# Optimization experiments

Hardware: AMD Instinct MI355X
Metric: run time of the kernel (lower is better)

The kernel has to match this reference:

```python
import jax, jax.numpy as jnp
import numpy as np

D_MODEL = 1024
N_HEADS = 16
HEAD_DIM = D_MODEL // N_HEADS
ROPE_BASE = 10000.0


def rotate_half(x):
    x1, x2 = x[..., : x.shape[-1] // 2], x[..., x.shape[-1] // 2 :]
    return jnp.concatenate((-x2, x1), axis=-1)


def rope_cos_sin(L, dim, dtype):
    inv_freq = 1.0 / (ROPE_BASE ** (jnp.arange(0, dim, 2, dtype=jnp.float32) / dim))
    freqs = jnp.arange(L, dtype=jnp.float32)[:, None] * inv_freq[None, :]  # [L, dim/2]
    emb = jnp.concatenate((freqs, freqs), axis=-1)  # [L, dim]
    # broadcast over batch and heads: [1, L, 1, dim]
    return jnp.cos(emb)[None, :, None, :].astype(dtype), jnp.sin(emb)[None, :, None, :].astype(dtype)


def setup_inputs() -> dict:
    key = jax.random.key(0)
    ks = jax.random.split(key, 11)
    N, L, S = 2, 2048, 2048
    s = 1.0 / np.sqrt(D_MODEL)
    return {
        "queries": jax.random.normal(ks[0], (N, L, D_MODEL), jnp.float32),
        "keys": jax.random.normal(ks[1], (N, S, D_MODEL), jnp.float32),
        "values": jax.random.normal(ks[2], (N, S, D_MODEL), jnp.float32),
        "Wq": jax.random.normal(ks[3], (D_MODEL, D_MODEL), jnp.float32) * s,
        "bq": jnp.zeros((D_MODEL,), jnp.float32),
        "Wk": jax.random.normal(ks[4], (D_MODEL, D_MODEL), jnp.float32) * s,
        "bk": jnp.zeros((D_MODEL,), jnp.float32),
        "Wv": jax.random.normal(ks[5], (D_MODEL, D_MODEL), jnp.float32) * s,
        "bv": jnp.zeros((D_MODEL,), jnp.float32),
        "Wo": jax.random.normal(ks[6], (D_MODEL, D_MODEL), jnp.float32) * s,
        "bo": jnp.zeros((D_MODEL,), jnp.float32),
    }


def reference(queries, keys, values, Wq, bq, Wk, bk, Wv, bv, Wo, bo):
    N, L, _ = queries.shape
    S = keys.shape[1]
    H, hd = N_HEADS, HEAD_DIM

    # QKV projections (nn.Linear: x @ W.T + b), reshape to [N, T, H, hd]
    q = (jnp.einsum("nld,ed->nle", queries, Wq) + bq).reshape(N, L, H, hd)
    k = (jnp.einsum("nsd,ed->nse", keys, Wk) + bk).reshape(N, S, H, hd)
    v = (jnp.einsum("nsd,ed->nse", values, Wv) + bv).reshape(N, S, H, hd)

    # Rotary embedding: q*cos + rotate_half(q)*sin  (same for k)
    cos, sin = rope_cos_sin(L, hd, q.dtype)
    q = q * cos + rotate_half(q) * sin
    k = k * cos + rotate_half(k) * sin

    # Inner attention: scaled dot-product with causal mask
    scores = jnp.einsum("nlhd,nshd->nhls", q, k) / jnp.sqrt(jnp.asarray(hd, q.dtype))
    causal = jnp.tril(jnp.ones((L, S), bool))
    scores = jnp.where(causal[None, None], scores, jnp.asarray(-1e9, scores.dtype))
    attn = jax.nn.softmax(scores, axis=-1)
    out = jnp.einsum("nhls,nshd->nlhd", attn, v).reshape(N, L, H * hd)

    # Output projection
    return jnp.einsum("nle,de->nld", out, Wo) + bo
```

## Files before the change

### kernel.cpp

```cpp
#include <hip/hip_runtime.h>
#include <math.h>

#define DM 1024
#define NH 16
#define HD 64
#define SEQ 2048
#define NB2 2
#define MROWS 4096

typedef unsigned short u16;
typedef __attribute__((ext_vector_type(8))) short short8;
typedef __attribute__((ext_vector_type(4))) float f32x4;
typedef __attribute__((ext_vector_type(2))) unsigned int u32x2;

#define GLOAD16(g, l) __builtin_amdgcn_global_load_lds( \
    (const __attribute__((address_space(1))) void*)(g),  \
    (__attribute__((address_space(3))) void*)(l), 16, 0, 0)

static __device__ __forceinline__ u16 f2bf(float f) {
  union { float f; unsigned u; } v; v.f = f;
  unsigned r = v.u + 0x7fffu + ((v.u >> 16) & 1u);
  return (u16)(r >> 16);
}

static __device__ __forceinline__ short8 cvt8(float4 a, float4 b) {
  short8 s;
  s[0] = (short)f2bf(a.x); s[1] = (short)f2bf(a.y);
  s[2] = (short)f2bf(a.z); s[3] = (short)f2bf(a.w);
  s[4] = (short)f2bf(b.x); s[5] = (short)f2bf(b.y);
  s[6] = (short)f2bf(b.z); s[7] = (short)f2bf(b.w);
  return s;
}

__global__ void conv_all(
    const float* __restrict__ q, const float* __restrict__ k, const float* __restrict__ v,
    const float* __restrict__ wq, const float* __restrict__ wk,
    const float* __restrict__ wv, const float* __restrict__ wo,
    u16* __restrict__ xq, u16* __restrict__ xk, u16* __restrict__ xv,
    u16* __restrict__ wqb, u16* __restrict__ wkb, u16* __restrict__ wvb, u16* __restrict__ wob,
    float* __restrict__ cosT, float* __restrict__ sinT)
{
  const int z = blockIdx.z;
  const int idx = blockIdx.x * blockDim.x + threadIdx.x;
  if (z == 7) {
    if (idx >= SEQ * 32) return;
    int l = idx >> 5, i = idx & 31;
    float invf = expf(-(float)i * (9.210340371976184f / 32.0f));
    float ang = (float)l * invf;
    float s, c;
    sincosf(ang, &s, &c);
    cosT[idx] = c; sinT[idx] = s;
    return;
  }
  const float* src; u16* dst; int n;
  switch (z) {
    case 0: src = q;  dst = xq;  n = MROWS * DM; break;
    case 1: src = k;  dst = xk;  n = MROWS * DM; break;
    case 2: src = v;  dst = xv;  n = MROWS * DM; break;
    case 3: src = wq; dst = wqb; n = DM * DM; break;
    case 4: src = wk; dst = wkb; n = DM * DM; break;
    case 5: src = wv; dst = wvb; n = DM * DM; break;
    default: src = wo; dst = wob; n = DM * DM; break;
  }
  const int base = idx * 8;
  if (base >= n) return;
  float4 a = *(const float4*)(src + base);
  float4 b = *(const float4*)(src + base + 4);
  *(short8*)(dst + base) = cvt8(a, b);
}

#define VSTR 136
template<int EPI>
__device__ __forceinline__ void gemm_body(
    u16* SH,
    const u16* __restrict__ A, const u16* __restrict__ W,
    const float* __restrict__ bias,
    u16* __restrict__ Cb, float* __restrict__ Cf, u16* __restrict__ VT,
    const float* __restrict__ cosT, const float* __restrict__ sinT,
    float qscale, int row0, int col0)
{
  const int tid = threadIdx.x;
  const int lane = tid & 63;
  const int wid = tid >> 6;
  const int wr = wid & 3;
  const int wc = wid >> 2;
  const int fr = lane & 15, kg = lane >> 4;

  const u16* ga = A + (size_t)(row0 + (tid & 127)) * DM + ((tid >> 7) << 3);
  const u16* gb = W + (size_t)(col0 + (tid & 127)) * DM + ((tid >> 7) << 3);
  const int lw = wid * 512;
  u16* B0 = SH;
  u16* B1 = SH + 16384;

  f32x4 acc[2][4];
#pragma unroll
  for (int m = 0; m < 2; ++m)
#pragma unroll
    for (int n = 0; n < 4; ++n) acc[m][n] = (f32x4){0.f, 0.f, 0.f, 0.f};

  auto issue = [&](int t, u16* buf) {
    const int ko = t * 64;
    GLOAD16(ga + ko, buf + lw);
    GLOAD16(ga + ko + 32, buf + lw + 4096);
    GLOAD16(gb + ko, buf + 8192 + lw);
    GLOAD16(gb + ko + 32, buf + 8192 + lw + 4096);
  };
  auto compute = [&](const u16* buf, int kk) {
    const int kc = kk * 4 + kg;
    short8 afr[2], bfr[4];
#pragma unroll
    for (int m = 0; m < 2; ++m)
      afr[m] = *(const short8*)(&buf[kc * 1024 + (wr * 32 + m * 16 + fr) * 8]);
#pragma unroll
    for (int n = 0; n < 4; ++n)
      bfr[n] = *(const short8*)(&buf[8192 + kc * 1024 + (wc * 64 + n * 16 + fr) * 8]);
    __builtin_amdgcn_s_setprio(1);
#pragma unroll
    for (int m = 0; m < 2; ++m)
#pragma unroll
      for (int n = 0; n < 4; ++n)
        acc[m][n] = __builtin_amdgcn_mfma_f32_16x16x32_bf16(afr[m], bfr[n], acc[m][n], 0, 0, 0);
    __builtin_amdgcn_s_setprio(0);
  };

  issue(0, B0);
  const int KT = DM / 64;
  for (int t = 0; t < KT; ++t) {
    u16* bufR = (t & 1) ? B1 : B0;
    u16* bufW = (t & 1) ? B0 : B1;
    __syncthreads();
    if (t + 1 < KT) issue(t + 1, bufW);
    compute(bufR, 0);
    compute(bufR, 1);
  }

  if (EPI == 2) {
    __syncthreads();
    const int nb = row0 >> 11;
    const int sbase = row0 & (SEQ - 1);
#pragma unroll
    for (int p = 0; p < 2; ++p) {
      if (wc == p) {
#pragma unroll
        for (int n = 0; n < 4; ++n) {
          const int dcol = n * 16 + fr;
          const float bv = bias[col0 + p * 64 + dcol];
#pragma unroll
          for (int m = 0; m < 2; ++m)
#pragma unroll
            for (int r = 0; r < 4; ++r)
              SH[dcol * VSTR + wr * 32 + m * 16 + kg * 4 + r] = f2bf(acc[m][n][r] + bv);
        }
      }
      __syncthreads();
      {
        const int dcol = tid >> 3, sq = tid & 7;
        const int e = col0 + p * 64 + dcol;
        u16* dst = VT + ((size_t)(nb * NH + (e >> 6)) * HD + (e & 63)) * SEQ + sbase + sq * 16;
        *(short8*)(dst)     = *(const short8*)(&SH[dcol * VSTR + sq * 16]);
        *(short8*)(dst + 8) = *(const short8*)(&SH[dcol * VSTR + sq * 16 + 8]);
      }
      __syncthreads();
    }
    return;
  }

#pragma unroll
  for (int m = 0; m < 2; ++m) {
#pragma unroll
    for (int r = 0; r < 4; ++r) {
      const int rowg = row0 + wr * 32 + m * 16 + kg * 4 + r;
      if (EPI == 1) {
#pragma unroll
        for (int n = 0; n < 4; ++n) {
          const int colg = col0 + wc * 64 + n * 16 + fr;
          Cf[(size_t)rowg * DM + colg] = acc[m][n][r] + bias[colg];
        }
      } else {
        const int l = rowg & (SEQ - 1);
#pragma unroll
        for (int n = 0; n < 4; ++n) {
          const int colg = col0 + wc * 64 + n * 16 + fr;
          const int i = n * 16 + fr;
          const int fi = i & 31;
          const float c = cosT[l * 32 + fi];
          const float s = sinT[l * 32 + fi];
          const float v = acc[m][n][r] + bias[colg];
          const float pv = acc[m][n ^ 2][r] + bias[col0 + wc * 64 + ((n ^ 2) * 16 + fr)];
          const float o = v * c + ((i < 32) ? -pv : pv) * s;
          Cb[(size_t)rowg * DM + colg] = f2bf(o * qscale);
        }
      }
    }
  }
}

__global__ __launch_bounds__(512) void gemm_qkv(
    const u16* __restrict__ Xq, const u16* __restrict__ Xk, const u16* __restrict__ Xv,
    const u16* __restrict__ Wqb, const u16* __restrict__ Wkb, const u16* __restrict__ Wvb,
    const float* __restrict__ bq, const float* __restrict__ bk, const float* __restrict__ bv,
    u16* __restrict__ Qb, u16* __restrict__ Kb, u16* __restrict__ VT,
    const float* __restrict__ cosT, const float* __restrict__ sinT)
{
  __shared__ __align__(16) u16 SH[32768];
  const int z = blockIdx.z;
  const int row0 = blockIdx.x * 128, col0 = blockIdx.y * 128;
  if (z == 2) {
    gemm_body<2>(SH, Xv, Wvb, bv, nullptr, nullptr, VT, nullptr, nullptr, 1.0f, row0, col0);
  } else if (z == 0) {
    gemm_body<0>(SH, Xq, Wqb, bq, Qb, nullptr, nullptr, cosT, sinT, 0.125f, row0, col0);
  } else {
    gemm_body<0>(SH, Xk, Wkb, bk, Kb, nullptr, nullptr, cosT, sinT, 1.0f, row0, col0);
  }
}

__global__ __launch_bounds__(512) void gemm_o(
    const u16* __restrict__ Ob, const u16* __restrict__ Wob,
    const float* __restrict__ bo, float* __restrict__ out)
{
  __shared__ __align__(16) u16 SH[32768];
  gemm_body<1>(SH, Ob, Wob, bo, nullptr, out, nullptr, nullptr, nullptr, 1.0f,
               blockIdx.x * 128, blockIdx.y * 128);
}

__global__ __launch_bounds__(512) void flash_attn(
    const u16* __restrict__ Qp, const u16* __restrict__ Kp,
    const u16* __restrict__ VT, u16* __restrict__ Op)
{
  __shared__ __align__(16) u16 Ks[4096];
  __shared__ __align__(16) u16 Vt[4096];
  __shared__ __align__(16) u16 Pl[9216];

  const int tid = threadIdx.x;
  const int lane = tid & 63;
  const int w = tid >> 6;
  const int fr = lane & 15, rg = lane >> 4;
  const int qbp = blockIdx.x;
  const int h = blockIdx.y, nb = blockIdx.z;

  const size_t headoff = (size_t)nb * SEQ * DM + (size_t)h * HD;
  const size_t vthead = (size_t)(nb * NH + h) * HD * SEQ;
  const int srow = tid >> 3;
  const int sch  = tid & 7;
  u16* Pw = &Pl[w * 1152];

  for (int pass = 0; pass < 2; ++pass) {
    const int qe = pass ? (15 - qbp) : qbp;
    const int KBend = 2 * qe + 2;
    const int qrow0 = qe * 128 + w * 16;
    const int qg = qrow0 + fr;

    short8 qf[2];
#pragma unroll
    for (int ck = 0; ck < 2; ++ck)
      qf[ck] = *(const short8*)(Qp + headoff + (size_t)(qrow0 + fr) * DM + ck * 32 + rg * 8);

    f32x4 accO[4];
#pragma unroll
    for (int df = 0; df < 4; ++df) accO[df] = (f32x4){0.f, 0.f, 0.f, 0.f};
    float m_run = -3e38f, l_run = 0.f;

    short8 kpf = *(const short8*)(Kp + headoff + (size_t)srow * DM + sch * 8);
    short8 vpf = *(const short8*)(VT + vthead + (size_t)srow * SEQ + sch * 8);

    for (int kb = 0; kb < KBend; ++kb) {
      *(short8*)(&Ks[(sch * 64 + (srow ^ sch)) * 8]) = kpf;
      *(short8*)(&Vt[(sch * 64 + (srow ^ sch)) * 8]) = vpf;
      __syncthreads();
      if (kb + 1 < KBend) {
        kpf = *(const short8*)(Kp + headoff + (size_t)((kb + 1) * 64 + srow) * DM + sch * 8);
        vpf = *(const short8*)(VT + vthead + (size_t)srow * SEQ + (kb + 1) * 64 + sch * 8);
      }

      const bool active = (kb * 64) <= (qrow0 + 15);
      if (active) {
        short8 kf[4][2];
#pragma unroll
        for (int sf = 0; sf < 4; ++sf)
#pragma unroll
          for (int ck = 0; ck < 2; ++ck) {
            const int dc = ck * 4 + rg;
            kf[sf][ck] = *(const short8*)(&Ks[(dc * 64 + ((sf * 16 + fr) ^ dc)) * 8]);
          }
        f32x4 sc_[4];
#pragma unroll
        for (int sf = 0; sf < 4; ++sf) {
          f32x4 z = (f32x4){0.f, 0.f, 0.f, 0.f};
#pragma unroll
          for (int ck = 0; ck < 2; ++ck)
            z = __builtin_amdgcn_mfma_f32_16x16x32_bf16(kf[sf][ck], qf[ck], z, 0, 0, 0);
          sc_[sf] = z;
        }
        float rowmax = -3e38f;
#pragma unroll
        for (int sf = 0; sf < 4; ++sf)
#pragma unroll
          for (int r = 0; r < 4; ++r) {
            const int sg = kb * 64 + sf * 16 + rg * 4 + r;
            float v = sc_[sf][r];
            v = (sg <= qg) ? v : -3e38f;
            sc_[sf][r] = v;
            rowmax = fmaxf(rowmax, v);
          }
        rowmax = fmaxf(rowmax, __shfl_xor(rowmax, 16, 64));
        rowmax = fmaxf(rowmax, __shfl_xor(rowmax, 32, 64));
        const float mnew = fmaxf(m_run, rowmax);
        const float scl = __expf(m_run - mnew);
        m_run = mnew;
        float psum = 0.f;
#pragma unroll
        for (int sf = 0; sf < 4; ++sf)
#pragma unroll
          for (int r = 0; r < 4; ++r) {
            const float p = __expf(sc_[sf][r] - mnew);
            sc_[sf][r] = p;
            psum += p;
          }
        psum += __shfl_xor(psum, 16, 64);
        psum += __shfl_xor(psum, 32, 64);
        l_run = l_run * scl + psum;
        const float s0 = __shfl(scl, rg * 4 + 0, 64);
        const float s1 = __shfl(scl, rg * 4 + 1, 64);
        const float s2 = __shfl(scl, rg * 4 + 2, 64);
        const float s3 = __shfl(scl, rg * 4 + 3, 64);
#pragma unroll
        for (int df = 0; df < 4; ++df) {
          accO[df][0] *= s0; accO[df][1] *= s1;
          accO[df][2] *= s2; accO[df][3] *= s3;
        }
#pragma unroll
        for (int sf = 0; sf < 4; ++sf) {
          u32x2 pv;
          pv[0] = (unsigned)f2bf(sc_[sf][0]) | ((unsigned)f2bf(sc_[sf][1]) << 16);
          pv[1] = (unsigned)f2bf(sc_[sf][2]) | ((unsigned)f2bf(sc_[sf][3]) << 16);
          *(u32x2*)(&Pw[fr * 72 + (sf * 8 + rg * 2) * 2]) = pv;
        }
        short8 pa[2];
#pragma unroll
        for (int ck = 0; ck < 2; ++ck)
          pa[ck] = *(const short8*)(&Pw[fr * 72 + (ck * 16 + rg * 4) * 2]);
#pragma unroll
        for (int df = 0; df < 4; ++df)
#pragma unroll
          for (int ck = 0; ck < 2; ++ck) {
            const int sc = ck * 4 + rg;
            const short8 vf = *(const short8*)(&Vt[(sc * 64 + ((df * 16 + fr) ^ sc)) * 8]);
            accO[df] = __builtin_amdgcn_mfma_f32_16x16x32_bf16(pa[ck], vf, accO[df], 0, 0, 0);
          }
      }
      __syncthreads();
    }

    const float l0 = __shfl(l_run, rg * 4 + 0, 64);
    const float l1 = __shfl(l_run, rg * 4 + 1, 64);
    const float l2 = __shfl(l_run, rg * 4 + 2, 64);
    const float l3 = __shfl(l_run, rg * 4 + 3, 64);
#pragma unroll
    for (int df = 0; df < 4; ++df) {
      const int d = df * 16 + fr;
      Op[headoff + (size_t)(qrow0 + rg * 4 + 0) * DM + d] = f2bf(accO[df][0] / l0);
      Op[headoff + (size_t)(qrow0 + rg * 4 + 1) * DM + d] = f2bf(accO[df][1] / l1);
      Op[headoff + (size_t)(qrow0 + rg * 4 + 2) * DM + d] = f2bf(accO[df][2] / l2);
      Op[headoff + (size_t)(qrow0 + rg * 4 + 3) * DM + d] = f2bf(accO[df][3] / l3);
    }
  }
}

extern "C" void kernel_launch(void* const* d_in, const int* in_sizes, int n_in,
                              void* d_out, int out_size, void* d_ws, size_t ws_size,
                              hipStream_t stream) {
  (void)in_sizes; (void)n_in; (void)out_size; (void)ws_size;
  const float* queries = (const float*)d_in[0];
  const float* keys    = (const float*)d_in[1];
  const float* values  = (const float*)d_in[2];
  const float* Wq = (const float*)d_in[3];
  const float* bq = (const float*)d_in[4];
  const float* Wk = (const float*)d_in[5];
  const float* bk = (const float*)d_in[6];
  const float* Wv = (const float*)d_in[7];
  const float* bv = (const float*)d_in[8];
  const float* Wo = (const float*)d_in[9];
  const float* bo = (const float*)d_in[10];
  float* out = (float*)d_out;

  char* ws = (char*)d_ws;
  const size_t MB = 1u << 20;
  u16* Qb  = (u16*)(ws);
  u16* Kb  = (u16*)(ws + 8 * MB);
  u16* VTg = (u16*)(ws + 16 * MB);
  u16* Xq  = (u16*)(ws + 24 * MB);
  u16* Ob  = Xq;
  u16* Xk  = (u16*)(ws + 32 * MB);
  u16* Xv  = (u16*)(ws + 40 * MB);
  u16* Wqb = (u16*)(ws + 48 * MB);
  u16* Wkb = (u16*)(ws + 50 * MB);
  u16* Wvb = (u16*)(ws + 52 * MB);
  u16* Wob = (u16*)(ws + 54 * MB);
  float* cosT = (float*)(ws + 56 * MB);
  float* sinT = (float*)(ws + 56 * MB + 256 * 1024);

  conv_all<<<dim3(2048, 1, 8), 256, 0, stream>>>(
      queries, keys, values, Wq, Wk, Wv, Wo,
      Xq, Xk, Xv, Wqb, Wkb, Wvb, Wob, cosT, sinT);
  gemm_qkv<<<dim3(MROWS / 128, DM / 128, 3), 512, 0, stream>>>(
      Xq, Xk, Xv, Wqb, Wkb, Wvb, bq, bk, bv, Qb, Kb, VTg, cosT, sinT);
  flash_attn<<<dim3(SEQ / 256, NH, NB2), 512, 0, stream>>>(Qb, Kb, VTg, Ob);
  gemm_o<<<dim3(MROWS / 128, DM / 128), 512, 0, stream>>>(Ob, Wob, bo, out);
}
```

Before: 149.4 us.

## Use 256x256 tiles with triple-buffered LDS pipeline for QKV GEMM

The QKV projection kernel moves from 128x128 to 256x256 output tiles, with each wave computing 128x64 using 8x4 MFMA accumulators, and k-steps of 32. It adds a three-buffer global_load_lds pipeline with explicit vmcnt waits and raw s_barrier so two tiles stay in flight. The goal is more data reuse per LDS load and less global traffic. In exchange the grid shrinks to 16x4x3=192 blocks (below CU count), register pressure rises, and LDS use grows to 96KB.

```diff
diff --git a/kernel.cpp b/kernel.cpp
--- a/kernel.cpp
+++ b/kernel.cpp
@@ -69,16 +69,155 @@
   *(short8*)(dst + base) = cvt8(a, b);
 }
 
-#define VSTR 136
-template<int EPI>
-__device__ __forceinline__ void gemm_body(
-    u16* SH,
-    const u16* __restrict__ A, const u16* __restrict__ W,
-    const float* __restrict__ bias,
-    u16* __restrict__ Cb, float* __restrict__ Cf, u16* __restrict__ VT,
-    const float* __restrict__ cosT, const float* __restrict__ sinT,
-    float qscale, int row0, int col0)
+__global__ __launch_bounds__(512) void gemm_qkv(
+    const u16* __restrict__ Xq, const u16* __restrict__ Xk, const u16* __restrict__ Xv,
+    const u16* __restrict__ Wqb, const u16* __restrict__ Wkb, const u16* __restrict__ Wvb,
+    const float* __restrict__ bq, const float* __restrict__ bk, const float* __restrict__ bv,
+    u16* __restrict__ Qb, u16* __restrict__ Kb, u16* __restrict__ VT,
+    const float* __restrict__ cosT, const float* __restrict__ sinT)
 {
+  __shared__ __align__(16) u16 SH[49152];
+  const int z = blockIdx.z;
+  const u16* A = (z == 0) ? Xq : (z == 1) ? Xk : Xv;
+  const u16* W = (z == 0) ? Wqb : (z == 1) ? Wkb : Wvb;
+  const float* bias = (z == 0) ? bq : (z == 1) ? bk : bv;
+  const int row0 = blockIdx.x * 256, col0 = blockIdx.y * 256;
+
+  const int tid = threadIdx.x;
+  const int lane = tid & 63;
+  const int wid = tid >> 6;
+  const int wm = wid >> 2;
+  const int wn = wid & 3;
+  const int fr = lane & 15, kg = lane >> 4;
+
+  const u16* ga = A + (size_t)(row0 + (tid & 255)) * DM + ((tid >> 8) << 3);
+  const u16* gb = W + (size_t)(col0 + (tid & 255)) * DM + ((tid >> 8) << 3);
+  const int lw = (wid >> 2) * 2048 + (wid & 3) * 512;
+  u16* B0 = SH;
+  u16* B1 = SH + 16384;
+  u16* B2 = SH + 32768;
+
+  f32x4 acc[8][4];
+#pragma unroll
+  for (int m = 0; m < 8; ++m)
+#pragma unroll
+    for (int n = 0; n < 4; ++n) acc[m][n] = (f32x4){0.f, 0.f, 0.f, 0.f};
+
+  auto issue = [&](int t, u16* buf) {
+    const int ko = t * 32;
+    GLOAD16(ga + ko, buf + lw);
+    GLOAD16(ga + ko + 16, buf + lw + 4096);
+    GLOAD16(gb + ko, buf + 8192 + lw);
+    GLOAD16(gb + ko + 16, buf + 8192 + lw + 4096);
+  };
+  auto compute = [&](const u16* buf) {
+    short8 afr[8], bfr[4];
+#pragma unroll
+    for (int m = 0; m < 8; ++m)
+      afr[m] = *(const short8*)(&buf[kg * 2048 + (wm * 128 + m * 16 + fr) * 8]);
+#pragma unroll
+    for (int n = 0; n < 4; ++n)
+      bfr[n] = *(const short8*)(&buf[8192 + kg * 2048 + (wn * 64 + n * 16 + fr) * 8]);
+    __builtin_amdgcn_s_setprio(1);
+#pragma unroll
+    for (int m = 0; m < 8; ++m)
+#pragma unroll
+      for (int n = 0; n < 4; ++n)
+        acc[m][n] = __builtin_amdgcn_mfma_f32_16x16x32_bf16(afr[m], bfr[n], acc[m][n], 0, 0, 0);
+    __builtin_amdgcn_s_setprio(0);
+  };
+
+  issue(0, B0);
+  issue(1, B1);
+
+#define STEP4(t, bufR, bufW) do {                                   \
+    asm volatile("s_waitcnt vmcnt(4)" ::: "memory");                \
+    __builtin_amdgcn_sched_barrier(0);                              \
+    __builtin_amdgcn_s_barrier();                                   \
+    __builtin_amdgcn_sched_barrier(0);                              \
+    if ((t) + 2 < 32) issue((t) + 2, bufW);                         \
+    compute(bufR);                                                  \
+  } while (0)
+#define STEP0(t, bufR) do {                                         \
+    asm volatile("s_waitcnt vmcnt(0)" ::: "memory");                \
+    __builtin_amdgcn_sched_barrier(0);                              \
+    __builtin_amdgcn_s_barrier();                                   \
+    __builtin_amdgcn_sched_barrier(0);                              \
+    compute(bufR);                                                  \
+  } while (0)
+
+  for (int t = 0; t < 30; t += 3) {
+    STEP4(t,     B0, B2);
+    STEP4(t + 1, B1, B0);
+    STEP4(t + 2, B2, B1);
+  }
+  STEP4(30, B0, B2);
+  STEP0(31, B1);
+#undef STEP4
+#undef STEP0
+
+  if (z == 2) {
+    __syncthreads();
+    const int nb = row0 >> 11;
+    const int sbase = row0 & (SEQ - 1);
+#pragma unroll
+    for (int p = 0; p < 4; ++p) {
+      if (wn == p) {
+#pragma unroll
+        for (int n = 0; n < 4; ++n) {
+          const int dcol = n * 16 + fr;
+          const float bv = bias[col0 + p * 64 + dcol];
+#pragma unroll
+          for (int m = 0; m < 8; ++m)
+#pragma unroll
+            for (int r = 0; r < 4; ++r)
+              SH[dcol * 264 + wm * 128 + m * 16 + kg * 4 + r] = f2bf(acc[m][n][r] + bv);
+        }
+      }
+      __syncthreads();
+      {
+        const int dcol = tid >> 3, sq = tid & 7;
+        const int e = col0 + p * 64 + dcol;
+        u16* dst = VT + ((size_t)(nb * NH + (e >> 6)) * HD + (e & 63)) * SEQ + sbase + sq * 32;
+#pragma unroll
+        for (int j = 0; j < 4; ++j)
+          *(short8*)(dst + j * 8) = *(const short8*)(&SH[dcol * 264 + sq * 32 + j * 8]);
+      }
+      __syncthreads();
+    }
+    return;
+  }
+
+  const float qscale = (z == 0) ? 0.125f : 1.0f;
+  u16* Cb = (z == 0) ? Qb : Kb;
+#pragma unroll
+  for (int m = 0; m < 8; ++m) {
+#pragma unroll
+    for (int r = 0; r < 4; ++r) {
+      const int rowg = row0 + wm * 128 + m * 16 + kg * 4 + r;
+      const int l = rowg & (SEQ - 1);
+#pragma unroll
+      for (int n = 0; n < 4; ++n) {
+        const int colg = col0 + wn * 64 + n * 16 + fr;
+        const int i = n * 16 + fr;
+        const int fi = i & 31;
+        const float c = cosT[l * 32 + fi];
+        const float s = sinT[l * 32 + fi];
+        const float v = acc[m][n][r] + bias[colg];
+        const float pv = acc[m][n ^ 2][r] + bias[col0 + wn * 64 + ((n ^ 2) * 16 + fr)];
+        const float o = v * c + ((i < 32) ? -pv : pv) * s;
+        Cb[(size_t)rowg * DM + colg] = f2bf(o * qscale);
+      }
+    }
+  }
+}
+
+__global__ __launch_bounds__(512) void gemm_o(
+    const u16* __restrict__ Ob, const u16* __restrict__ Wob,
+    const float* __restrict__ bo, float* __restrict__ out)
+{
+  __shared__ __align__(16) u16 SH[32768];
+  const int row0 = blockIdx.x * 128, col0 = blockIdx.y * 128;
   const int tid = threadIdx.x;
   const int lane = tid & 63;
   const int wid = tid >> 6;
@@ -86,8 +225,8 @@
   const int wc = wid >> 2;
   const int fr = lane & 15, kg = lane >> 4;
 
-  const u16* ga = A + (size_t)(row0 + (tid & 127)) * DM + ((tid >> 7) << 3);
-  const u16* gb = W + (size_t)(col0 + (tid & 127)) * DM + ((tid >> 7) << 3);
+  const u16* ga = Ob + (size_t)(row0 + (tid & 127)) * DM + ((tid >> 7) << 3);
+  const u16* gb = Wob + (size_t)(col0 + (tid & 127)) * DM + ((tid >> 7) << 3);
   const int lw = wid * 512;
   u16* B0 = SH;
   u16* B1 = SH + 16384;
@@ -134,93 +273,18 @@
     compute(bufR, 1);
   }
 
-  if (EPI == 2) {
-    __syncthreads();
-    const int nb = row0 >> 11;
-    const int sbase = row0 & (SEQ - 1);
-#pragma unroll
-    for (int p = 0; p < 2; ++p) {
-      if (wc == p) {
-#pragma unroll
-        for (int n = 0; n < 4; ++n) {
-          const int dcol = n * 16 + fr;
-          const float bv = bias[col0 + p * 64 + dcol];
-#pragma unroll
-          for (int m = 0; m < 2; ++m)
-#pragma unroll
-            for (int r = 0; r < 4; ++r)
-              SH[dcol * VSTR + wr * 32 + m * 16 + kg * 4 + r] = f2bf(acc[m][n][r] + bv);
-        }
-      }
-      __syncthreads();
-      {
-        const int dcol = tid >> 3, sq = tid & 7;
-        const int e = col0 + p * 64 + dcol;
-        u16* dst = VT + ((size_t)(nb * NH + (e >> 6)) * HD + (e & 63)) * SEQ + sbase + sq * 16;
-        *(short8*)(dst)     = *(const short8*)(&SH[dcol * VSTR + sq * 16]);
-        *(short8*)(dst + 8) = *(const short8*)(&SH[dcol * VSTR + sq * 16 + 8]);
-      }
-      __syncthreads();
-    }
-    return;
-  }
-
 #pragma unroll
   for (int m = 0; m < 2; ++m) {
 #pragma unroll
     for (int r = 0; r < 4; ++r) {
       const int rowg = row0 + wr * 32 + m * 16 + kg * 4 + r;
-      if (EPI == 1) {
-#pragma unroll
-        for (int n = 0; n < 4; ++n) {
-          const int colg = col0 + wc * 64 + n * 16 + fr;
-          Cf[(size_t)rowg * DM + colg] = acc[m][n][r] + bias[colg];
-        }
-      } else {
-        const int l = rowg & (SEQ - 1);
-#pragma unroll
-        for (int n = 0; n < 4; ++n) {
-          const int colg = col0 + wc * 64 + n * 16 + fr;
-          const int i = n * 16 + fr;
-          const int fi = i & 31;
-          const float c = cosT[l * 32 + fi];
-          const float s = sinT[l * 32 + fi];
-          const float v = acc[m][n][r] + bias[colg];
-          const float pv = acc[m][n ^ 2][r] + bias[col0 + wc * 64 + ((n ^ 2) * 16 + fr)];
-          const float o = v * c + ((i < 32) ? -pv : pv) * s;
-          Cb[(size_t)rowg * DM + colg] = f2bf(o * qscale);
-        }
+#pragma unroll
+      for (int n = 0; n < 4; ++n) {
+        const int colg = col0 + wc * 64 + n * 16 + fr;
+        out[(size_t)rowg * DM + colg] = acc[m][n][r] + bo[colg];
       }
     }
   }
-}
-
-__global__ __launch_bounds__(512) void gemm_qkv(
-    const u16* __restrict__ Xq, const u16* __restrict__ Xk, const u16* __restrict__ Xv,
-    const u16* __restrict__ Wqb, const u16* __restrict__ Wkb, const u16* __restrict__ Wvb,
-    const float* __restrict__ bq, const float* __restrict__ bk, const float* __restrict__ bv,
-    u16* __restrict__ Qb, u16* __restrict__ Kb, u16* __restrict__ VT,
-    const float* __restrict__ cosT, const float* __restrict__ sinT)
-{
-  __shared__ __align__(16) u16 SH[32768];
-  const int z = blockIdx.z;
-  const int row0 = blockIdx.x * 128, col0 = blockIdx.y * 128;
-  if (z == 2) {
-    gemm_body<2>(SH, Xv, Wvb, bv, nullptr, nullptr, VT, nullptr, nullptr, 1.0f, row0, col0);
-  } else if (z == 0) {
-    gemm_body<0>(SH, Xq, Wqb, bq, Qb, nullptr, nullptr, cosT, sinT, 0.125f, row0, col0);
-  } else {
-    gemm_body<0>(SH, Xk, Wkb, bk, Kb, nullptr, nullptr, cosT, sinT, 1.0f, row0, col0);
-  }
-}
-
-__global__ __launch_bounds__(512) void gemm_o(
-    const u16* __restrict__ Ob, const u16* __restrict__ Wob,
-    const float* __restrict__ bo, float* __restrict__ out)
-{
-  __shared__ __align__(16) u16 SH[32768];
-  gemm_body<1>(SH, Ob, Wob, bo, nullptr, out, nullptr, nullptr, nullptr, 1.0f,
-               blockIdx.x * 128, blockIdx.y * 128);
 }
 
 __global__ __launch_bounds__(512) void flash_attn(
@@ -402,7 +466,7 @@
   conv_all<<<dim3(2048, 1, 8), 256, 0, stream>>>(
       queries, keys, values, Wq, Wk, Wv, Wo,
       Xq, Xk, Xv, Wqb, Wkb, Wvb, Wob, cosT, sinT);
-  gemm_qkv<<<dim3(MROWS / 128, DM / 128, 3), 512, 0, stream>>>(
+  gemm_qkv<<<dim3(MROWS / 256, DM / 256, 3), 512, 0, stream>>>(
       Xq, Xk, Xv, Wqb, Wkb, Wvb, bq, bk, bv, Qb, Kb, VTg, cosT, sinT);
   flash_attn<<<dim3(SEQ / 256, NH, NB2), 512, 0, stream>>>(Qb, Kb, VTg, Ob);
   gemm_o<<<dim3(MROWS / 128, DM / 128), 512, 0, stream>>>(Ob, Wob, bo, out);
```

Measured after the change: 148.4 us. Within noise of the previous version (-0.7%).
